# Kernel tuning notes

Measured on AMD Instinct MI355X. Metric: run time of the kernel, lower is better.

The kernel has to match this reference:

```python
import jax, jax.numpy as jnp
import numpy as np

POS_TH = 0.5
NEG_TH = 0.4
NEGPOS_RATIO = 3
BBOX_ALPHA = 1.5
CONF_ALPHA = 1.0
VAR_CXCY = 0.1
VAR_WH = 0.2
NUM_CLASSES = 41
B, P, G = 8, 100000, 16


def setup_inputs() -> dict:
    key = jax.random.key(0)
    k = jax.random.split(key, 8)
    loc_data = jax.random.normal(k[0], (B, P, 4), dtype=jnp.float32)
    conf_data = jax.random.normal(k[1], (B, P, NUM_CLASSES), dtype=jnp.float32)
    # priors in (cx, cy, w, h), normalized coords
    p_cxy = jax.random.uniform(k[2], (P, 2), minval=0.0, maxval=1.0)
    p_wh = jax.random.uniform(k[3], (P, 2), minval=0.02, maxval=0.3)
    priors = jnp.concatenate([p_cxy, p_wh], axis=1).astype(jnp.float32)
    # gt boxes in point form (x1, y1, x2, y2)
    g_cxy = jax.random.uniform(k[4], (B, G, 2), minval=0.15, maxval=0.85)
    g_wh = jax.random.uniform(k[5], (B, G, 2), minval=0.05, maxval=0.4)
    gt_boxes = jnp.concatenate([
        jnp.clip(g_cxy - g_wh / 2, 0.0, 1.0),
        jnp.clip(g_cxy + g_wh / 2, 0.0, 1.0),
    ], axis=-1).astype(jnp.float32)
    gt_labels = jax.random.randint(k[6], (B, G), 1, NUM_CLASSES)
    return {"loc_data": loc_data, "conf_data": conf_data, "priors": priors,
            "gt_boxes": gt_boxes, "gt_labels": gt_labels}


def point_form(pr):
    return jnp.concatenate([pr[:, :2] - pr[:, 2:] / 2,
                            pr[:, :2] + pr[:, 2:] / 2], axis=1)


def jaccard(a, b):
    # a: [G,4] xyxy, b: [P,4] xyxy -> [G,P]
    lt = jnp.maximum(a[:, None, :2], b[None, :, :2])
    rb = jnp.minimum(a[:, None, 2:], b[None, :, 2:])
    wh = jnp.clip(rb - lt, 0.0)
    inter = wh[..., 0] * wh[..., 1]
    area_a = ((a[:, 2] - a[:, 0]) * (a[:, 3] - a[:, 1]))[:, None]
    area_b = ((b[:, 2] - b[:, 0]) * (b[:, 3] - b[:, 1]))[None, :]
    return inter / (area_a + area_b - inter)


def encode(matched, priors):
    # matched [P,4] xyxy, priors [P,4] cxcywh -> SSD offsets with variances
    g_cxcy = ((matched[:, :2] + matched[:, 2:]) / 2 - priors[:, :2]) / (VAR_CXCY * priors[:, 2:])
    g_wh = jnp.log(jnp.clip((matched[:, 2:] - matched[:, :2]) / priors[:, 2:], 1e-8)) / VAR_WH
    return jnp.concatenate([g_cxcy, g_wh], axis=1)


def match_one(gt_box, gt_label, priors):
    # gt_box [G,4], gt_label [G], priors [P,4] -> loc_t [P,4], conf_t [P]
    pf = point_form(priors)
    ov = jaccard(gt_box, pf)                      # [G,P]
    best_truth_ov = ov.max(axis=0)                # [P]
    best_truth_idx = ov.argmax(axis=0)            # [P]
    best_prior_idx = ov.argmax(axis=1)            # [G] best prior per gt
    # force-match each gt to its best prior
    best_truth_ov = best_truth_ov.at[best_prior_idx].set(2.0)
    best_truth_idx = best_truth_idx.at[best_prior_idx].set(jnp.arange(gt_box.shape[0]))
    conf = gt_label[best_truth_idx]
    conf = jnp.where(best_truth_ov < POS_TH, -1, conf)   # neutral
    conf = jnp.where(best_truth_ov < NEG_TH, 0, conf)    # background
    loc = encode(gt_box[best_truth_idx], priors)
    return loc, conf


def reference(loc_data, conf_data, priors, gt_boxes, gt_labels):
    bsz, n_pri, n_cls = conf_data.shape
    loc_t, conf_t = jax.vmap(match_one, in_axes=(0, 0, None))(gt_boxes, gt_labels, priors)
    pos = conf_t > 0                               # [B,P]
    num_pos = pos.sum(axis=1)                      # [B]
    # pos_weights: uniform 1/num_pos per image (ones split then normalized)
    pos_w = pos.astype(loc_data.dtype) / jnp.clip(num_pos, 1).astype(loc_data.dtype)[:, None]
    # localization: weighted SmoothL1 over positives
    d = loc_data - loc_t
    sl1 = jnp.where(jnp.abs(d) < 1.0, 0.5 * d * d, jnp.abs(d) - 0.5)
    loss_B = (pos_w[..., None] * sl1).sum() * BBOX_ALPHA
    # OHEM hard negative mining on background-suppression loss
    loss_c = jax.nn.logsumexp(conf_data, axis=-1) - conf_data[..., 0]
    loss_c = jnp.where(pos | (conf_t < 0), 0.0, loss_c)
    order = jnp.argsort(-loss_c, axis=1)
    rank = jnp.argsort(order, axis=1)
    num_neg = jnp.clip(NEGPOS_RATIO * num_pos, 0, n_pri - 1)
    neg = (rank < num_neg[:, None]) & (~pos) & (conf_t >= 0)
    keep = (pos | neg).astype(conf_data.dtype)
    logp = jax.nn.log_softmax(conf_data, axis=-1)
    ce = -jnp.take_along_axis(logp, jnp.clip(conf_t, 0)[..., None], axis=-1)[..., 0]
    total_pos = jnp.clip(num_pos.sum(), 1).astype(conf_data.dtype)
    loss_C = (ce * keep).sum() * CONF_ALPHA / total_pos
    return (loss_B + loss_C) / bsz
```

## Files before the change

### kernel.cpp

```cpp
#include <hip/hip_runtime.h>
#include <stdint.h>

#define BATCH 8
#define NPRI 100000
#define NGT 16
#define NCLS 41
#define F_POS_TH 0.5f
#define F_NEG_TH 0.4f

static constexpr int WTPB = 64;
static constexpr int CPT = WTPB * NCLS / 4;
static constexpr int BLK_PER_B = 224;
static constexpr int TILES_PER_B = (NPRI + WTPB - 1) / WTPB;
static constexpr int H0BIN = 256;
static constexpr int NBIN = 4096;

static constexpr size_t OFF_KEY  = 0;
static constexpr size_t OFF_GTC  = OFF_KEY + (size_t)BATCH*NPRI*4;
static constexpr size_t OFF_HG   = OFF_GTC + BATCH*NGT*8;
static constexpr size_t OFF_NPOS = OFF_HG + (size_t)BATCH*H0BIN*4;
static constexpr size_t OFF_SL1  = OFF_NPOS + BATCH*4;
static constexpr size_t OFF_CEP  = OFF_SL1  + BATCH*4;
static constexpr size_t OFF_NEG  = OFF_CEP  + BATCH*4;
static constexpr size_t OFF_FTK  = OFF_NEG  + BATCH*4;
static constexpr int ZERO_U32 = (int)((OFF_FTK + 4 - OFF_HG) / 4);

typedef float f32x4 __attribute__((ext_vector_type(4)));

__device__ inline float smoothl1(float d) {
  float a = fabsf(d);
  return a < 1.f ? 0.5f * d * d : a - 0.5f;
}
__device__ inline float sl1_terms(f32x4 pv, f32x4 ld, f32x4 gv) {
  float tx = ((gv[0] + gv[2]) * 0.5f - pv[0]) / (0.1f * pv[2]);
  float ty = ((gv[1] + gv[3]) * 0.5f - pv[1]) / (0.1f * pv[3]);
  float tw = __logf(fmaxf((gv[2] - gv[0]) / pv[2], 1e-8f)) / 0.2f;
  float th = __logf(fmaxf((gv[3] - gv[1]) / pv[3], 1e-8f)) / 0.2f;
  return smoothl1(ld[0] - tx) + smoothl1(ld[1] - ty)
       + smoothl1(ld[2] - tw) + smoothl1(ld[3] - th);
}
__device__ inline float aload_f32(const float* p) {
  return __hip_atomic_load(p, __ATOMIC_RELAXED, __HIP_MEMORY_SCOPE_AGENT);
}
__device__ inline unsigned aload_u32(const unsigned* p) {
  return __hip_atomic_load(p, __ATOMIC_RELAXED, __HIP_MEMORY_SCOPE_AGENT);
}
__device__ __forceinline__ void gll16(const void* gsrc, void* ldst) {
  __builtin_amdgcn_global_load_lds(
      (const __attribute__((address_space(1))) void*)gsrc,
      (__attribute__((address_space(3))) void*)ldst, 16, 0, 0);
}

__global__ void k_init(unsigned* __restrict__ z, unsigned long long* __restrict__ gtc) {
  int t = threadIdx.x;
  for (int i = t; i < ZERO_U32; i += 512) z[i] = 0u;
  if (t < BATCH * NGT) gtc[t] = 0xFFFFFFFFull;
}

__global__ __launch_bounds__(WTPB) void k_conf(
    const float* __restrict__ loc, const float* __restrict__ conf,
    const float* __restrict__ priors, const float* __restrict__ gtb,
    const int* __restrict__ gtl,
    unsigned* __restrict__ key, unsigned* __restrict__ histg,
    unsigned long long* __restrict__ gtc,
    unsigned* __restrict__ npos, float* __restrict__ sl1sum, float* __restrict__ cepos) {
  __shared__ float buf[2][CPT * 4];
  __shared__ unsigned hcb[H0BIN];
  __shared__ unsigned long long best[NGT];
  int t = threadIdx.x;
  int b = blockIdx.x / BLK_PER_B;
  int sub = blockIdx.x % BLK_PER_B;
  const f32x4* conf4 = (const f32x4*)conf;
  const size_t bbase4 = (size_t)b * NPRI * NCLS / 4;
  const size_t maxc4 = (size_t)BATCH * NPRI * NCLS / 4 - 1;
  float acc_s = 0.f, acc_c = 0.f; unsigned acc_p = 0;
#pragma unroll
  for (int u = 0; u < H0BIN / WTPB; u++) hcb[t + u * WTPB] = 0u;
  if (t < NGT) best[t] = 0;

  {
    size_t base4 = bbase4 + (size_t)sub * CPT;
#pragma unroll
    for (int u = 0; u < 10; u++) {
      size_t g4 = base4 + (unsigned)(t + u * WTPB);
      if (g4 > maxc4) g4 = maxc4;
      gll16(conf4 + g4, &buf[0][(t + u * WTPB) * 4]);
    }
    if (t < CPT - 10 * WTPB) {
      size_t g4 = base4 + (unsigned)(t + 10 * WTPB);
      if (g4 > maxc4) g4 = maxc4;
      gll16(conf4 + g4, &buf[0][(t + 10 * WTPB) * 4]);
    }
  }
  int cur = 0;
  for (int tidx = sub; tidx < TILES_PER_B; tidx += BLK_PER_B) {
    int p = tidx * WTPB + t;
    bool valid = p < NPRI;
    int pc = valid ? p : NPRI - 1;
    f32x4 pv = ((const f32x4*)priors)[pc];
    f32x4 ld = ((const f32x4*)loc)[(size_t)b * NPRI + pc];
    int nxt = tidx + BLK_PER_B;
    if (nxt < TILES_PER_B) {
      size_t base4 = bbase4 + (size_t)nxt * CPT;
#pragma unroll
      for (int u = 0; u < 10; u++) {
        size_t g4 = base4 + (unsigned)(t + u * WTPB);
        if (g4 > maxc4) g4 = maxc4;
        gll16(conf4 + g4, &buf[cur ^ 1][(t + u * WTPB) * 4]);
      }
      if (t < CPT - 10 * WTPB) {
        size_t g4 = base4 + (unsigned)(t + 10 * WTPB);
        if (g4 > maxc4) g4 = maxc4;
        gll16(conf4 + g4, &buf[cur ^ 1][(t + 10 * WTPB) * 4]);
      }
      __builtin_amdgcn_sched_barrier(0);
      asm volatile("s_waitcnt vmcnt(11)");
      __builtin_amdgcn_sched_barrier(0);
    } else {
      __builtin_amdgcn_sched_barrier(0);
      asm volatile("s_waitcnt vmcnt(0)");
      __builtin_amdgcn_sched_barrier(0);
    }
    unsigned kkreg = 0u;
    if (valid) {
      float px1 = pv[0] - 0.5f * pv[2], py1 = pv[1] - 0.5f * pv[3];
      float px2 = pv[0] + 0.5f * pv[2], py2 = pv[1] + 0.5f * pv[3];
      float parea = (px2 - px1) * (py2 - py1);
      float bov = 0.f; int g = 0;
#pragma unroll
      for (int gg = 0; gg < NGT; gg++) {
        const f32x4 gv = ((const f32x4*)gtb)[b * NGT + gg];
        float ix = fmaxf(fminf(px2, gv[2]) - fmaxf(px1, gv[0]), 0.f);
        float iy = fmaxf(fminf(py2, gv[3]) - fmaxf(py1, gv[1]), 0.f);
        float inter = ix * iy;
        float garea = (gv[2] - gv[0]) * (gv[3] - gv[1]);
        float iou = inter / (parea + garea - inter);
        if (iou > bov) { bov = iou; g = gg; }
        if (iou > 0.f) {
          unsigned long long comp = ((unsigned long long)__float_as_uint(iou) << 32)
                                  | (unsigned long long)(0xFFFFFFFFu - (unsigned)p);
          if (comp > best[gg]) atomicMax(&best[gg], comp);
        }
      }
      int c = gtl[b * NGT + g];
      if (bov < F_POS_TH) c = -1;
      if (bov < F_NEG_TH) c = 0;
      const float* r = &buf[cur][t * NCLS];
      float s = 0.f, r0 = 0.f, rc = 0.f;
#pragma unroll
      for (int j = 0; j < NCLS; j++) {
        float v = r[j];
        s += __expf(v);
        if (j == 0) r0 = v;
        if (j == c) rc = v;
      }
      float lse = __logf(s);
      kkreg = (c == 0) ? __float_as_uint(lse - r0) : 0u;
      key[(size_t)b * NPRI + p] = kkreg;
      if (c > 0) {
        acc_p += 1;
        acc_c += lse - rc;
        const f32x4 gvb = ((const f32x4*)gtb)[b * NGT + g];
        acc_s += sl1_terms(pv, ld, gvb);
      }
    }
    unsigned bin = kkreg >> 24;
    unsigned long long m40 = __ballot(valid && kkreg != 0u && bin == 0x40u);
    unsigned long long m00 = __ballot(valid && kkreg == 0u);
    if (m40 && t == __ffsll((long long)m40) - 1)
      atomicAdd(&hcb[0x40], (unsigned)__popcll(m40));
    if (m00 && t == __ffsll((long long)m00) - 1)
      atomicAdd(&hcb[0], (unsigned)__popcll(m00));
    if (valid && kkreg != 0u && bin != 0x40u) atomicAdd(&hcb[bin], 1u);
    cur ^= 1;
  }
  if (t < NGT && best[t] != 0) atomicMax(&gtc[b * NGT + t], best[t]);
#pragma unroll
  for (int u = 0; u < H0BIN / WTPB; u++) {
    unsigned v = hcb[t + u * WTPB];
    if (v) atomicAdd(&histg[b * H0BIN + t + u * WTPB], v);
  }
  float vs = acc_s, vc = acc_c; unsigned vp = acc_p;
#pragma unroll
  for (int off = 32; off; off >>= 1) {
    vs += __shfl_down(vs, off, 64);
    vc += __shfl_down(vc, off, 64);
    vp += __shfl_down(vp, off, 64);
  }
  if (t == 0) {
    if (vp) atomicAdd(&npos[b], vp);
    if (vs != 0.f) atomicAdd(&sl1sum[b], vs);
    if (vc != 0.f) atomicAdd(&cepos[b], vc);
  }
}

__global__ __launch_bounds__(1024) void k_select(
    const float* __restrict__ loc, const float* __restrict__ conf,
    const float* __restrict__ priors, const float* __restrict__ gtb,
    const int* __restrict__ gtl, const unsigned long long* __restrict__ gtc,
    unsigned* __restrict__ key, const unsigned* __restrict__ histg,
    unsigned* __restrict__ npos, float* __restrict__ sl1sum,
    float* __restrict__ cepos, float* __restrict__ negsum,
    unsigned* __restrict__ final_tk, float* __restrict__ out) {
  __shared__ unsigned hc[NBIN];
  __shared__ unsigned h0s[H0BIN];
  __shared__ unsigned pcs[256], sc[256];
  __shared__ int wA; __shared__ unsigned kexA;
  __shared__ unsigned kS, prefS;
  __shared__ float redf[16];
  __shared__ unsigned pw16[NGT];
  int b = blockIdx.x, t = threadIdx.x;
  if (t < H0BIN) h0s[t] = histg[b * H0BIN + t];
  if (t < NGT)
    pw16[t] = 0xFFFFFFFFu - (unsigned)(gtc[b * NGT + t] & 0xFFFFFFFFull);
  if (t == 0) { kS = 0u; prefS = 0u; wA = -1; }
  __syncthreads();
  float d_sl = 0.f, d_ce = 0.f; int d_np = 0;
  if (t < NGT) {
    unsigned p = pw16[t];
    bool is_first = true, is_last = true;
    for (int j = 0; j < NGT; j++) {
      if (j < t && pw16[j] == p) is_first = false;
      if (j > t && pw16[j] == p) is_last = false;
    }
    const float* row = conf + ((size_t)b * NPRI + p) * NCLS;
    float s = 0.f;
    for (int j = 0; j < NCLS; j++) s += __expf(row[j]);
    float lse = __logf(s);
    f32x4 pv = ((const f32x4*)priors)[p];
    f32x4 ldv = ((const f32x4*)loc)[(size_t)b * NPRI + p];
    if (is_first) {
      float px1 = pv[0] - 0.5f * pv[2], py1 = pv[1] - 0.5f * pv[3];
      float px2 = pv[0] + 0.5f * pv[2], py2 = pv[1] + 0.5f * pv[3];
      float parea = (px2 - px1) * (py2 - py1);
      float bov = 0.f; int gold = 0;
      for (int gg = 0; gg < NGT; gg++) {
        const f32x4 gv = ((const f32x4*)gtb)[b * NGT + gg];
        float ix = fmaxf(fminf(px2, gv[2]) - fmaxf(px1, gv[0]), 0.f);
        float iy = fmaxf(fminf(py2, gv[3]) - fmaxf(py1, gv[1]), 0.f);
        float inter = ix * iy;
        float garea = (gv[2] - gv[0]) * (gv[3] - gv[1]);
        float iou = inter / (parea + garea - inter);
        if (iou > bov) { bov = iou; gold = gg; }
      }
      int cold = (bov < F_NEG_TH) ? 0 : ((bov < F_POS_TH) ? -1 : gtl[b * NGT + gold]);
      if (cold == 0) {
        unsigned ko = key[(size_t)b * NPRI + p];
        atomicSub(&h0s[ko >> 24], 1u);
        atomicAdd(&h0s[0], 1u);
      } else if (cold > 0) {
        d_np -= 1;
        d_ce -= lse - row[cold];
        d_sl -= sl1_terms(pv, ldv, ((const f32x4*)gtb)[b * NGT + gold]);
      }
      d_np += 1;
      key[(size_t)b * NPRI + p] = 0u;
    }
    if (is_last) {
      d_ce += lse - row[gtl[b * NGT + t]];
      d_sl += sl1_terms(pv, ldv, ((const f32x4*)gtb)[b * NGT + t]);
    }
  }
  if (t < 64) {
    float vs = d_sl, vc = d_ce; int vp = d_np;
#pragma unroll
    for (int off = 32; off; off >>= 1) {
      vs += __shfl_down(vs, off, 64);
      vc += __shfl_down(vc, off, 64);
      vp += __shfl_down(vp, off, 64);
    }
    if (t == 0) {
      npos[b] = (unsigned)((int)npos[b] + vp);
      sl1sum[b] += vs;
      cepos[b] += vc;
    }
  }
  __syncthreads();
  unsigned k0 = min(3u * npos[b], (unsigned)(NPRI - 1));
  const int iters = (NPRI + 1023) / 1024;
  if (t < 256) { unsigned v = h0s[t]; pcs[t] = v; sc[t] = v; }
  __syncthreads();
  for (int off = 1; off < 256; off <<= 1) {
    unsigned v = 0;
    if (t < 256) v = (t + off < 256) ? sc[t + off] : 0u;
    __syncthreads();
    if (t < 256) sc[t] += v;
    __syncthreads();
  }
  if (t < 256) {
    unsigned excl = sc[t] - pcs[t];
    if (k0 > 0 && excl < k0 && k0 <= excl + pcs[t]) { wA = t; kexA = excl; }
  }
  __syncthreads();
  if (t == 0 && wA >= 0) { prefS = ((unsigned)wA) << 24; kS = k0 - kexA; }
  __syncthreads();
  for (int lvl = 1; lvl <= 2; lvl++) {
    unsigned k = kS;
    int shift = (lvl == 1) ? 12 : 0;
    int lowcut = (lvl == 1) ? 24 : 12;
    for (int i = t; i < NBIN; i += 1024) hc[i] = 0u;
    if (t == 0) wA = -1;
    __syncthreads();
    unsigned pre = prefS >> lowcut;
    if (k > 0) {
      for (int n = 0; n < iters; n++) {
        int i = n * 1024 + t;
        if (i < NPRI) {
          unsigned kk = key[(size_t)b * NPRI + i];
          if ((kk >> lowcut) == pre) atomicAdd(&hc[(kk >> shift) & 0xFFFu], 1u);
        }
      }
    }
    __syncthreads();
    if (t < 256) {
      unsigned cs = 0;
#pragma unroll
      for (int u = 0; u < 16; u++) cs += hc[t * 16 + u];
      pcs[t] = cs; sc[t] = cs;
    }
    __syncthreads();
    for (int off = 1; off < 256; off <<= 1) {
      unsigned v = 0;
      if (t < 256) v = (t + off < 256) ? sc[t + off] : 0u;
      __syncthreads();
      if (t < 256) sc[t] += v;
      __syncthreads();
    }
    if (t < 256) {
      unsigned excl = sc[t] - pcs[t];
      if (k > 0 && excl < k && k <= excl + pcs[t]) { wA = t; kexA = excl; }
    }
    __syncthreads();
    if (wA >= 0 && t < 64) {
      int w = wA; unsigned exw = kexA;
      unsigned v = (t < 16) ? hc[w * 16 + t] : 0u;
      unsigned sufv = v;
#pragma unroll
      for (int off = 1; off < 16; off <<= 1) {
        unsigned x = __shfl_down(sufv, off, 64);
        if (t + off < 16) sufv += x;
      }
      unsigned excl2 = exw + (sufv - v);
      if (t < 16 && excl2 < k && k <= excl2 + v) {
        prefS |= ((unsigned)(w * 16 + t)) << shift;
        kS = k - excl2;
      }
    }
    __syncthreads();
  }
  unsigned Tu = prefS;
  unsigned tie = kS;
  float acc = 0.f;
  if (k0 > 0) {
    for (int n = 0; n < iters; n++) {
      int i = n * 1024 + t;
      if (i < NPRI) {
        unsigned kk = key[(size_t)b * NPRI + i];
        if (kk > Tu) acc += __uint_as_float(kk);
      }
    }
  }
#pragma unroll
  for (int off = 32; off; off >>= 1) acc += __shfl_down(acc, off, 64);
  if ((t & 63) == 0) redf[t >> 6] = acc;
  __syncthreads();
  if (t == 0) {
    float tot = 0.f;
    for (int wv = 0; wv < 16; wv++) tot += redf[wv];
    if (k0 > 0) tot += (float)tie * __uint_as_float(Tu);
    negsum[b] = tot;
    __threadfence();
    unsigned r2 = atomicAdd(final_tk, 1u);
    if (r2 == BATCH - 1) {
      __threadfence();
      float lb = 0.f, ctot = 0.f; unsigned tp = 0;
      for (int bb = 0; bb < BATCH; bb++) {
        unsigned nb = aload_u32(&npos[bb]);
        lb += aload_f32(&sl1sum[bb]) / fmaxf((float)nb, 1.f);
        tp += nb;
        ctot += aload_f32(&cepos[bb]) + aload_f32(&negsum[bb]);
      }
      out[0] = (1.5f * lb + ctot / fmaxf((float)tp, 1.f)) / (float)BATCH;
      *final_tk = 0;
    }
  }
}

extern "C" void kernel_launch(void* const* d_in, const int* in_sizes, int n_in,
                              void* d_out, int out_size, void* d_ws, size_t ws_size,
                              hipStream_t stream) {
  const float* loc = (const float*)d_in[0];
  const float* conf = (const float*)d_in[1];
  const float* priors = (const float*)d_in[2];
  const float* gtb = (const float*)d_in[3];
  const int* gtl = (const int*)d_in[4];
  char* ws = (char*)d_ws;
  unsigned* key = (unsigned*)(ws + OFF_KEY);
  unsigned long long* gtc = (unsigned long long*)(ws + OFF_GTC);
  unsigned* histg = (unsigned*)(ws + OFF_HG);
  unsigned* npos = (unsigned*)(ws + OFF_NPOS);
  float* sl1sum = (float*)(ws + OFF_SL1);
  float* cepos = (float*)(ws + OFF_CEP);
  float* negsum = (float*)(ws + OFF_NEG);
  unsigned* final_tk = (unsigned*)(ws + OFF_FTK);
  float* out = (float*)d_out;

  k_init<<<1, 512, 0, stream>>>(histg, gtc);
  k_conf<<<BATCH * BLK_PER_B, WTPB, 0, stream>>>(loc, conf, priors, gtb, gtl,
                                                 key, histg, gtc, npos, sl1sum, cepos);
  k_select<<<BATCH, 1024, 0, stream>>>(loc, conf, priors, gtb, gtl, gtc,
                                       key, histg, npos, sl1sum, cepos,
                                       negsum, final_tk, out);
}
```

Before: 159.4 us.

## Replace persistent LDS-pipelined conf kernel with one-thread-per-prior direct loads

The persistent 64-thread blocks, which double-buffered conf tiles into LDS with global_load_lds, are replaced by a 2D grid of 256-thread blocks. Each thread handles one prior and loads its 41-float conf row directly into registers as vector loads. The class logit for positives is re-read from global memory, and per-block reductions go through shared memory across four waves. This removes the manual pipelining and LDS traffic and raises parallelism. The cost is strided, poorly coalesced per-lane row loads that are not 16-byte aligned, which now depend on cache reuse.

New measurement: 169.9 us. 1.07x slower.

```diff
diff --git a/kernel.cpp b/kernel.cpp
--- a/kernel.cpp
+++ b/kernel.cpp
@@ -8,10 +8,8 @@
 #define F_POS_TH 0.5f
 #define F_NEG_TH 0.4f
 
-static constexpr int WTPB = 64;
-static constexpr int CPT = WTPB * NCLS / 4;
-static constexpr int BLK_PER_B = 224;
-static constexpr int TILES_PER_B = (NPRI + WTPB - 1) / WTPB;
+static constexpr int CTPB = 256;
+static constexpr int CBLK = (NPRI + CTPB - 1) / CTPB;
 static constexpr int H0BIN = 256;
 static constexpr int NBIN = 4096;
 
@@ -45,11 +43,6 @@
 __device__ inline unsigned aload_u32(const unsigned* p) {
   return __hip_atomic_load(p, __ATOMIC_RELAXED, __HIP_MEMORY_SCOPE_AGENT);
 }
-__device__ __forceinline__ void gll16(const void* gsrc, void* ldst) {
-  __builtin_amdgcn_global_load_lds(
-      (const __attribute__((address_space(1))) void*)gsrc,
-      (__attribute__((address_space(3))) void*)ldst, 16, 0, 0);
-}
 
 __global__ void k_init(unsigned* __restrict__ z, unsigned long long* __restrict__ gtc) {
   int t = threadIdx.x;
@@ -57,140 +50,123 @@
   if (t < BATCH * NGT) gtc[t] = 0xFFFFFFFFull;
 }
 
-__global__ __launch_bounds__(WTPB) void k_conf(
+__global__ __launch_bounds__(CTPB) void k_conf(
     const float* __restrict__ loc, const float* __restrict__ conf,
     const float* __restrict__ priors, const float* __restrict__ gtb,
     const int* __restrict__ gtl,
     unsigned* __restrict__ key, unsigned* __restrict__ histg,
     unsigned long long* __restrict__ gtc,
     unsigned* __restrict__ npos, float* __restrict__ sl1sum, float* __restrict__ cepos) {
-  __shared__ float buf[2][CPT * 4];
   __shared__ unsigned hcb[H0BIN];
   __shared__ unsigned long long best[NGT];
-  int t = threadIdx.x;
-  int b = blockIdx.x / BLK_PER_B;
-  int sub = blockIdx.x % BLK_PER_B;
-  const f32x4* conf4 = (const f32x4*)conf;
-  const size_t bbase4 = (size_t)b * NPRI * NCLS / 4;
-  const size_t maxc4 = (size_t)BATCH * NPRI * NCLS / 4 - 1;
-  float acc_s = 0.f, acc_c = 0.f; unsigned acc_p = 0;
-#pragma unroll
-  for (int u = 0; u < H0BIN / WTPB; u++) hcb[t + u * WTPB] = 0u;
+  __shared__ float redS[4], redC[4]; __shared__ unsigned redP[4];
+  const int t = threadIdx.x, w = t >> 6, l = t & 63;
+  const int b = blockIdx.y;
+  const int p = blockIdx.x * CTPB + t;
+  const bool valid = p < NPRI;
+  const int pc = valid ? p : NPRI - 1;
+  hcb[t] = 0u;
   if (t < NGT) best[t] = 0;
-
-  {
-    size_t base4 = bbase4 + (size_t)sub * CPT;
-#pragma unroll
-    for (int u = 0; u < 10; u++) {
-      size_t g4 = base4 + (unsigned)(t + u * WTPB);
-      if (g4 > maxc4) g4 = maxc4;
-      gll16(conf4 + g4, &buf[0][(t + u * WTPB) * 4]);
-    }
-    if (t < CPT - 10 * WTPB) {
-      size_t g4 = base4 + (unsigned)(t + 10 * WTPB);
-      if (g4 > maxc4) g4 = maxc4;
-      gll16(conf4 + g4, &buf[0][(t + 10 * WTPB) * 4]);
-    }
-  }
-  int cur = 0;
-  for (int tidx = sub; tidx < TILES_PER_B; tidx += BLK_PER_B) {
-    int p = tidx * WTPB + t;
-    bool valid = p < NPRI;
-    int pc = valid ? p : NPRI - 1;
-    f32x4 pv = ((const f32x4*)priors)[pc];
-    f32x4 ld = ((const f32x4*)loc)[(size_t)b * NPRI + pc];
-    int nxt = tidx + BLK_PER_B;
-    if (nxt < TILES_PER_B) {
-      size_t base4 = bbase4 + (size_t)nxt * CPT;
-#pragma unroll
-      for (int u = 0; u < 10; u++) {
-        size_t g4 = base4 + (unsigned)(t + u * WTPB);
-        if (g4 > maxc4) g4 = maxc4;
-        gll16(conf4 + g4, &buf[cur ^ 1][(t + u * WTPB) * 4]);
-      }
-      if (t < CPT - 10 * WTPB) {
-        size_t g4 = base4 + (unsigned)(t + 10 * WTPB);
-        if (g4 > maxc4) g4 = maxc4;
-        gll16(conf4 + g4, &buf[cur ^ 1][(t + 10 * WTPB) * 4]);
-      }
-      __builtin_amdgcn_sched_barrier(0);
-      asm volatile("s_waitcnt vmcnt(11)");
-      __builtin_amdgcn_sched_barrier(0);
-    } else {
-      __builtin_amdgcn_sched_barrier(0);
-      asm volatile("s_waitcnt vmcnt(0)");
-      __builtin_amdgcn_sched_barrier(0);
-    }
-    unsigned kkreg = 0u;
-    if (valid) {
-      float px1 = pv[0] - 0.5f * pv[2], py1 = pv[1] - 0.5f * pv[3];
-      float px2 = pv[0] + 0.5f * pv[2], py2 = pv[1] + 0.5f * pv[3];
-      float parea = (px2 - px1) * (py2 - py1);
-      float bov = 0.f; int g = 0;
-#pragma unroll
-      for (int gg = 0; gg < NGT; gg++) {
-        const f32x4 gv = ((const f32x4*)gtb)[b * NGT + gg];
-        float ix = fmaxf(fminf(px2, gv[2]) - fmaxf(px1, gv[0]), 0.f);
-        float iy = fmaxf(fminf(py2, gv[3]) - fmaxf(py1, gv[1]), 0.f);
-        float inter = ix * iy;
-        float garea = (gv[2] - gv[0]) * (gv[3] - gv[1]);
-        float iou = inter / (parea + garea - inter);
-        if (iou > bov) { bov = iou; g = gg; }
-        if (iou > 0.f) {
-          unsigned long long comp = ((unsigned long long)__float_as_uint(iou) << 32)
-                                  | (unsigned long long)(0xFFFFFFFFu - (unsigned)p);
-          if (comp > best[gg]) atomicMax(&best[gg], comp);
-        }
-      }
-      int c = gtl[b * NGT + g];
-      if (bov < F_POS_TH) c = -1;
-      if (bov < F_NEG_TH) c = 0;
-      const float* r = &buf[cur][t * NCLS];
-      float s = 0.f, r0 = 0.f, rc = 0.f;
-#pragma unroll
-      for (int j = 0; j < NCLS; j++) {
-        float v = r[j];
-        s += __expf(v);
-        if (j == 0) r0 = v;
-        if (j == c) rc = v;
-      }
-      float lse = __logf(s);
-      kkreg = (c == 0) ? __float_as_uint(lse - r0) : 0u;
-      key[(size_t)b * NPRI + p] = kkreg;
-      if (c > 0) {
-        acc_p += 1;
-        acc_c += lse - rc;
-        const f32x4 gvb = ((const f32x4*)gtb)[b * NGT + g];
-        acc_s += sl1_terms(pv, ld, gvb);
-      }
-    }
-    unsigned bin = kkreg >> 24;
-    unsigned long long m40 = __ballot(valid && kkreg != 0u && bin == 0x40u);
-    unsigned long long m00 = __ballot(valid && kkreg == 0u);
-    if (m40 && t == __ffsll((long long)m40) - 1)
-      atomicAdd(&hcb[0x40], (unsigned)__popcll(m40));
-    if (m00 && t == __ffsll((long long)m00) - 1)
-      atomicAdd(&hcb[0], (unsigned)__popcll(m00));
-    if (valid && kkreg != 0u && bin != 0x40u) atomicAdd(&hcb[bin], 1u);
-    cur ^= 1;
-  }
+  __syncthreads();
+  float accS = 0.f, accC = 0.f; unsigned accP = 0;
+  const float* row = conf + ((size_t)b * NPRI + pc) * NCLS;
+  f32x4 a0 = *(const f32x4*)(row + 0);
+  f32x4 a1 = *(const f32x4*)(row + 4);
+  f32x4 a2 = *(const f32x4*)(row + 8);
+  f32x4 a3 = *(const f32x4*)(row + 12);
+  f32x4 a4 = *(const f32x4*)(row + 16);
+  f32x4 a5 = *(const f32x4*)(row + 20);
+  f32x4 a6 = *(const f32x4*)(row + 24);
+  f32x4 a7 = *(const f32x4*)(row + 28);
+  f32x4 a8 = *(const f32x4*)(row + 32);
+  f32x4 a9 = *(const f32x4*)(row + 36);
+  float a40 = row[40];
+  const f32x4 pv = ((const f32x4*)priors)[pc];
+  const f32x4 ld = ((const f32x4*)loc)[(size_t)b * NPRI + pc];
+  float px1 = pv[0] - 0.5f * pv[2], py1 = pv[1] - 0.5f * pv[3];
+  float px2 = pv[0] + 0.5f * pv[2], py2 = pv[1] + 0.5f * pv[3];
+  float parea = (px2 - px1) * (py2 - py1);
+  float bov = 0.f; int g = 0;
+#pragma unroll
+  for (int gg = 0; gg < NGT; gg++) {
+    const f32x4 gv = ((const f32x4*)gtb)[b * NGT + gg];
+    float ix = fmaxf(fminf(px2, gv[2]) - fmaxf(px1, gv[0]), 0.f);
+    float iy = fmaxf(fminf(py2, gv[3]) - fmaxf(py1, gv[1]), 0.f);
+    float inter = ix * iy;
+    float garea = (gv[2] - gv[0]) * (gv[3] - gv[1]);
+    float iou = inter / (parea + garea - inter);
+    if (iou > bov) { bov = iou; g = gg; }
+    if (valid && iou > 0.f) {
+      unsigned long long comp = ((unsigned long long)__float_as_uint(iou) << 32)
+                              | (unsigned long long)(0xFFFFFFFFu - (unsigned)p);
+      if (comp > best[gg]) atomicMax(&best[gg], comp);
+    }
+  }
+  float s = 0.f;
+#pragma unroll
+  for (int e = 0; e < 4; e++) s += __expf(a0[e]);
+#pragma unroll
+  for (int e = 0; e < 4; e++) s += __expf(a1[e]);
+#pragma unroll
+  for (int e = 0; e < 4; e++) s += __expf(a2[e]);
+#pragma unroll
+  for (int e = 0; e < 4; e++) s += __expf(a3[e]);
+#pragma unroll
+  for (int e = 0; e < 4; e++) s += __expf(a4[e]);
+#pragma unroll
+  for (int e = 0; e < 4; e++) s += __expf(a5[e]);
+#pragma unroll
+  for (int e = 0; e < 4; e++) s += __expf(a6[e]);
+#pragma unroll
+  for (int e = 0; e < 4; e++) s += __expf(a7[e]);
+#pragma unroll
+  for (int e = 0; e < 4; e++) s += __expf(a8[e]);
+#pragma unroll
+  for (int e = 0; e < 4; e++) s += __expf(a9[e]);
+  s += __expf(a40);
+  float lse = __logf(s);
+  unsigned kkreg = 0u;
+  if (valid) {
+    int c = gtl[b * NGT + g];
+    if (bov < F_POS_TH) c = -1;
+    if (bov < F_NEG_TH) c = 0;
+    kkreg = (c == 0) ? __float_as_uint(lse - a0[0]) : 0u;
+    key[(size_t)b * NPRI + p] = kkreg;
+    if (c > 0) {
+      accP = 1;
+      float rc = conf[((size_t)b * NPRI + p) * NCLS + c];
+      accC = lse - rc;
+      const f32x4 gvb = ((const f32x4*)gtb)[b * NGT + g];
+      accS = sl1_terms(pv, ld, gvb);
+    }
+  }
+  unsigned bin = kkreg >> 24;
+  unsigned long long m40 = __ballot(valid && kkreg != 0u && bin == 0x40u);
+  unsigned long long m00 = __ballot(valid && kkreg == 0u);
+  if (m40 && l == __ffsll((long long)m40) - 1)
+    atomicAdd(&hcb[0x40], (unsigned)__popcll(m40));
+  if (m00 && l == __ffsll((long long)m00) - 1)
+    atomicAdd(&hcb[0], (unsigned)__popcll(m00));
+  if (valid && kkreg != 0u && bin != 0x40u) atomicAdd(&hcb[bin], 1u);
+  __syncthreads();
   if (t < NGT && best[t] != 0) atomicMax(&gtc[b * NGT + t], best[t]);
-#pragma unroll
-  for (int u = 0; u < H0BIN / WTPB; u++) {
-    unsigned v = hcb[t + u * WTPB];
-    if (v) atomicAdd(&histg[b * H0BIN + t + u * WTPB], v);
-  }
-  float vs = acc_s, vc = acc_c; unsigned vp = acc_p;
+  { unsigned v = hcb[t]; if (v) atomicAdd(&histg[b * H0BIN + t], v); }
+  float vs = accS, vc = accC; unsigned vp = accP;
 #pragma unroll
   for (int off = 32; off; off >>= 1) {
     vs += __shfl_down(vs, off, 64);
     vc += __shfl_down(vc, off, 64);
     vp += __shfl_down(vp, off, 64);
   }
+  if (l == 0) { redS[w] = vs; redC[w] = vc; redP[w] = vp; }
+  __syncthreads();
   if (t == 0) {
-    if (vp) atomicAdd(&npos[b], vp);
-    if (vs != 0.f) atomicAdd(&sl1sum[b], vs);
-    if (vc != 0.f) atomicAdd(&cepos[b], vc);
+    float ts = redS[0] + redS[1] + redS[2] + redS[3];
+    float tc = redC[0] + redC[1] + redC[2] + redC[3];
+    unsigned tp = redP[0] + redP[1] + redP[2] + redP[3];
+    if (tp) atomicAdd(&npos[b], tp);
+    if (ts != 0.f) atomicAdd(&sl1sum[b], ts);
+    if (tc != 0.f) atomicAdd(&cepos[b], tc);
   }
 }
 
@@ -406,8 +382,9 @@
   float* out = (float*)d_out;
 
   k_init<<<1, 512, 0, stream>>>(histg, gtc);
-  k_conf<<<BATCH * BLK_PER_B, WTPB, 0, stream>>>(loc, conf, priors, gtb, gtl,
-                                                 key, histg, gtc, npos, sl1sum, cepos);
+  dim3 gridC(CBLK, BATCH);
+  k_conf<<<gridC, CTPB, 0, stream>>>(loc, conf, priors, gtb, gtl,
+                                     key, histg, gtc, npos, sl1sum, cepos);
   k_select<<<BATCH, 1024, 0, stream>>>(loc, conf, priors, gtb, gtl, gtc,
                                        key, histg, npos, sl1sum, cepos,
                                        negsum, final_tk, out);
```
